# Performance work log

Hardware: AMD Instinct MI355X
Metric: run time of the kernel (lower is better)

Reference implementation:

```python
import jax, jax.numpy as jnp
import numpy as np

B, C, T = 8, 1024, 2048
CI = C // 2
BN_EPS = 1e-5


def setup_inputs() -> dict:
    key = jax.random.key(0)
    ks = jax.random.split(key, 12)
    sc_in = 1.0 / np.sqrt(C)
    sc_ci = 1.0 / np.sqrt(CI)
    return {
        "x": jax.random.normal(ks[0], (B, C, T), dtype=jnp.float32),
        "Wq_w": jax.random.normal(ks[1], (CI, C), dtype=jnp.float32) * sc_in,
        "Wq_b": jax.random.normal(ks[2], (CI,), dtype=jnp.float32) * 0.02,
        "Wk_w": jax.random.normal(ks[3], (CI, C), dtype=jnp.float32) * sc_in,
        "Wk_b": jax.random.normal(ks[4], (CI,), dtype=jnp.float32) * 0.02,
        "Wv_w": jax.random.normal(ks[5], (CI, C), dtype=jnp.float32) * sc_in,
        "Wv_b": jax.random.normal(ks[6], (CI,), dtype=jnp.float32) * 0.02,
        "Wo_w": jax.random.normal(ks[7], (C, CI), dtype=jnp.float32) * sc_ci,
        "Wo_b": jax.random.normal(ks[8], (C,), dtype=jnp.float32) * 0.02,
        "gamma": jax.random.normal(ks[9], (C,), dtype=jnp.float32) * 0.1 + 1.0,
        "beta": jax.random.normal(ks[10], (C,), dtype=jnp.float32) * 0.02,
    }


def reference(x, Wq_w, Wq_b, Wk_w, Wk_b, Wv_w, Wv_b, Wo_w, Wo_b, gamma, beta):
    # 1x1 Conv1d projections == channel-wise linear maps
    q = jnp.einsum('oc,bct->bto', Wq_w, x) + Wq_b          # [B, T, Ci]
    k = jnp.einsum('oc,bct->bot', Wk_w, x) + Wk_b[:, None]  # [B, Ci, T]
    v = jnp.einsum('oc,bct->bto', Wv_w, x) + Wv_b          # [B, T, Ci]

    s = jnp.einsum('bqc,bck->bqk', q, k)                   # [B, Tq, Tk], unscaled
    sim = jax.nn.softmax(s, axis=-2)                        # softmax over QUERY axis
    y = jnp.einsum('bqk,bkc->bcq', sim, v)                  # [B, Ci, T]

    wy = jnp.einsum('oc,bct->bot', Wo_w, y) + Wo_b[:, None]  # [B, C, T]

    # BatchNorm1d in training mode: stats over (batch, time) per channel
    mean = jnp.mean(wy, axis=(0, 2), keepdims=True)
    var = jnp.var(wy, axis=(0, 2), keepdims=True)
    wy_bn = (wy - mean) * jax.lax.rsqrt(var + BN_EPS)
    wy_bn = wy_bn * gamma[None, :, None] + beta[None, :, None]

    return wy_bn + x
```

## Files before the change

kernel.cpp:

```cpp
#include <hip/hip_runtime.h>
#include <hip/hip_fp16.h>

typedef _Float16 f16;
typedef f16 f16x8 __attribute__((ext_vector_type(8)));
typedef f16 f16x4 __attribute__((ext_vector_type(4)));
typedef float f32x4 __attribute__((ext_vector_type(4)));

constexpr int Bb = 8, Cc = 1024, Tt = 2048, Ci = 512;
constexpr float BN_EPS = 1e-5f;

__device__ __forceinline__ void gload16(const f16* g, f16* l) {
  __builtin_amdgcn_global_load_lds(
      (const __attribute__((address_space(1))) void*)g,
      (__attribute__((address_space(3))) void*)l, 16, 0, 0);
}

__global__ __launch_bounds__(256)
void cvt_kernel(const float* __restrict__ src, f16* __restrict__ dst, int n4) {
  int i = blockIdx.x * blockDim.x + threadIdx.x;
  if (i < n4) {
    float4 v = *((const float4*)src + i);
    f16x4 h;
    h[0] = (f16)v.x; h[1] = (f16)v.y; h[2] = (f16)v.z; h[3] = (f16)v.w;
    *((f16x4*)dst + i) = h;
  }
}

__global__ __launch_bounds__(256)
void cvtT_kernel(const float* __restrict__ x, f16* __restrict__ xT) {
  __shared__ float tile[64][68];
  const int b = blockIdx.z, c0 = blockIdx.y * 64, t0 = blockIdx.x * 64;
  const int tid = threadIdx.x;
  const float* xp = x + ((long)b * Cc + c0) * Tt + t0;
  {
    int r = tid >> 4, c4 = (tid & 15) * 4;
    #pragma unroll
    for (int it = 0; it < 4; it++) {
      float4 v = *(const float4*)(xp + (long)(r + it * 16) * Tt + c4);
      *(float4*)&tile[r + it * 16][c4] = v;
    }
  }
  __syncthreads();
  f16* op = xT + ((long)b * Tt + t0) * Cc + c0;
  {
    int c8 = (tid & 7) * 8;
    #pragma unroll
    for (int it = 0; it < 2; it++) {
      int t = (tid >> 3) + it * 32;
      f16x8 o;
      #pragma unroll
      for (int jj = 0; jj < 8; jj++) o[jj] = (f16)tile[c8 + jj][t];
      *(f16x8*)(op + (long)t * Cc + c8) = o;
    }
  }
}

template<int BIAS_MODE, bool DO_MAX>
__global__ __launch_bounds__(512, 2)
void gemm8p(const f16* __restrict__ A, const f16* __restrict__ B,
            f16* __restrict__ C, const float* __restrict__ bias,
            unsigned* __restrict__ gmax,
            int K, int lda, int ldb, int ldc, long sA, long sB, long sC,
            int nx, int ny)
{
  extern __shared__ f16 lds[];
  constexpr int TILE_A = 256 * 32;
  constexpr int TILE_B = 128 * 32;
  constexpr int TILE   = TILE_A + TILE_B;

  const int per = gridDim.x >> 3;
  const int nid = (blockIdx.x & 7) * per + (blockIdx.x >> 3);
  const int bz = nid / (nx * ny);
  const int rem = nid - bz * nx * ny;
  const int by = rem / nx, bx = rem - by * nx;

  const int tid = threadIdx.x, lane = tid & 63, wv = tid >> 6;
  const int bm0 = by * 256, bn0 = bx * 128;
  const int wm = (wv >> 1) * 64, wn = (wv & 1) * 64;
  const f16* Ab = A + (long)bz * sA + (long)bm0 * lda;
  const f16* Bt = B + (long)bz * sB + (long)bn0 * ldb;
  C += (long)bz * sC;

  const int r16 = lane & 15, khi = lane >> 4;

  auto stA = [&](int slot, int k0, int r) {
    int L = (r * 512 + tid) * 16;
    int G = L ^ (((L >> 7) & 3) << 4);
    gload16(Ab + (long)(G >> 6) * lda + k0 + ((G & 63) >> 1),
            lds + (long)slot * TILE + (r * 512 + wv * 64) * 8);
  };
  auto stB = [&](int slot, int k0) {
    int L = tid * 16;
    int G = L ^ (((L >> 7) & 3) << 4);
    gload16(Bt + (long)(G >> 6) * ldb + k0 + ((G & 63) >> 1),
            lds + (long)slot * TILE + TILE_A + (wv * 64) * 8);
  };

  f32x4 acc[4][4] = {};
  const int nt = K >> 5;

  stA(0, 0, 0); stA(0, 0, 1); stB(0, 0);
  stA(1, 32, 0); stA(1, 32, 1); stB(1, 32);
  asm volatile("s_waitcnt vmcnt(3)" ::: "memory");
  __builtin_amdgcn_s_barrier();

  for (int t = 0; t < nt; t++) {
    const int slot = t % 3;
    const int nslot = (t + 2) % 3;
    const int k2 = (t + 2) << 5;
    const bool st = (t + 2) < nt;
    const char* baseA = (const char*)(lds + (long)slot * TILE);
    const char* baseB = (const char*)(lds + (long)slot * TILE + TILE_A);

    if (st) { stA(nslot, k2, 0); stA(nslot, k2, 1); stB(nslot, k2); }

    f16x8 af[4], bf[4];
    #pragma unroll
    for (int i = 0; i < 4; i++) {
      const int row = wm + i * 16 + r16;
      af[i] = *(const f16x8*)(baseA + (((row << 6) + (khi << 4)) ^ (((row >> 1) & 3) << 4)));
    }
    #pragma unroll
    for (int j = 0; j < 4; j++) {
      const int row = wn + j * 16 + r16;
      bf[j] = *(const f16x8*)(baseB + (((row << 6) + (khi << 4)) ^ (((row >> 1) & 3) << 4)));
    }

    __builtin_amdgcn_s_setprio(1);
    #pragma unroll
    for (int i = 0; i < 4; i++)
      #pragma unroll
      for (int j = 0; j < 4; j++)
        acc[i][j] = __builtin_amdgcn_mfma_f32_16x16x32_f16(af[i], bf[j], acc[i][j], 0, 0, 0);
    __builtin_amdgcn_s_setprio(0);

    __builtin_amdgcn_sched_barrier(0);
    if (st) asm volatile("s_waitcnt vmcnt(3)" ::: "memory");
    else    asm volatile("s_waitcnt vmcnt(0)" ::: "memory");
    __builtin_amdgcn_s_barrier();
  }

  const int rg = khi * 4;
  float cmx[4] = {-3e38f, -3e38f, -3e38f, -3e38f};
  #pragma unroll
  for (int i = 0; i < 4; i++) {
    const int row0 = bm0 + wm + i * 16 + rg;
    #pragma unroll
    for (int r = 0; r < 4; r++) {
      const int row = row0 + r;
      const float br = (BIAS_MODE == 1) ? bias[row] : 0.0f;
      #pragma unroll
      for (int j = 0; j < 4; j++) {
        const int col = bn0 + wn + j * 16 + r16;
        float v = acc[i][j][r] + ((BIAS_MODE == 2) ? bias[col] : br);
        C[(long)row * ldc + col] = (f16)v;
        if (DO_MAX) cmx[j] = fmaxf(cmx[j], v);
      }
    }
  }
  if (DO_MAX) {
    #pragma unroll
    for (int j = 0; j < 4; j++) {
      float mx = cmx[j];
      mx = fmaxf(mx, __shfl_xor(mx, 16));
      mx = fmaxf(mx, __shfl_xor(mx, 32));
      if (khi == 0) {
        const int col = bn0 + wn + j * 16 + r16;
        unsigned u = __float_as_uint(mx);
        unsigned key = (u & 0x80000000u) ? ~u : (u | 0x80000000u);
        atomicMax(gmax + (long)bz * ldc + col, key);
      }
    }
  }
}

__global__ __launch_bounds__(256)
void colsum_kernel(f16* __restrict__ E, const unsigned* __restrict__ gmax,
                   float* __restrict__ sums) {
  const int b = blockIdx.z;
  const int kt = blockIdx.x * 256 + threadIdx.x;
  const long q0 = (long)blockIdx.y * 128;
  unsigned key = gmax[b * Tt + kt];
  float m = (key & 0x80000000u) ? __uint_as_float(key ^ 0x80000000u)
                                : __uint_as_float(~key);
  f16* p = E + ((long)b * Tt + q0) * Tt + kt;
  float s = 0.f;
  #pragma unroll 4
  for (int q = 0; q < 128; q++) {
    float e = __expf((float)p[(long)q * Tt] - m);
    p[(long)q * Tt] = (f16)e;
    s += e;
  }
  atomicAdd(sums + b * Tt + kt, s);
}

__global__ __launch_bounds__(256)
void vscale_kernel(f16* __restrict__ Vt, const float* __restrict__ sums) {
  long i = ((long)blockIdx.x * 256 + threadIdx.x) * 8;
  int kt = (int)(i & (Tt - 1));
  int b = (int)(i >> 20);
  f16x8 v = *(f16x8*)(Vt + i);
  const float* sp = sums + b * Tt + kt;
  #pragma unroll
  for (int j = 0; j < 8; j++)
    v[j] = (f16)((float)v[j] * __fdividef(1.0f, sp[j]));
  *(f16x8*)(Vt + i) = v;
}

__global__ __launch_bounds__(256)
void bnstat_kernel(const f16* __restrict__ wy, float* __restrict__ bsum,
                   float* __restrict__ bsq) {
  const int c = blockIdx.x, tid = threadIdx.x;
  float s1 = 0.f, s2 = 0.f;
  for (int b = 0; b < Bb; b++) {
    f16x8 v = *((const f16x8*)(wy + ((long)b * Cc + c) * Tt) + tid);
    #pragma unroll
    for (int jj = 0; jj < 8; jj++) { float f = (float)v[jj]; s1 += f; s2 += f * f; }
  }
  #pragma unroll
  for (int off = 1; off < 64; off <<= 1) {
    s1 += __shfl_xor(s1, off);
    s2 += __shfl_xor(s2, off);
  }
  __shared__ float l1[4], l2[4];
  const int w = tid >> 6;
  if ((tid & 63) == 0) { l1[w] = s1; l2[w] = s2; }
  __syncthreads();
  if (tid == 0) {
    bsum[c] = (l1[0] + l1[1]) + (l1[2] + l1[3]);
    bsq[c]  = (l2[0] + l2[1]) + (l2[2] + l2[3]);
  }
}

__global__ __launch_bounds__(256)
void final_kernel(const f16* __restrict__ wy, const float* __restrict__ x,
                  const float* __restrict__ gamma, const float* __restrict__ beta,
                  const float* __restrict__ bsum, const float* __restrict__ bsq,
                  float* __restrict__ out)
{
  long i = ((long)blockIdx.x * blockDim.x + threadIdx.x) * 4;
  int c = (int)((i >> 11) & (Cc - 1));
  const float cnt = (float)Bb * (float)Tt;
  float mean = bsum[c] / cnt;
  float var  = bsq[c] / cnt - mean * mean;
  float sc = rsqrtf(var + BN_EPS) * gamma[c];
  float sh = beta[c] - mean * sc;
  f16x4 w = *(const f16x4*)(wy + i);
  float4 xv = *(const float4*)(x + i);
  float4 o;
  o.x = (float)w[0] * sc + sh + xv.x;
  o.y = (float)w[1] * sc + sh + xv.y;
  o.z = (float)w[2] * sc + sh + xv.z;
  o.w = (float)w[3] * sc + sh + xv.w;
  *(float4*)(out + i) = o;
}

extern "C" void kernel_launch(void* const* d_in, const int* in_sizes, int n_in,
                              void* d_out, int out_size, void* d_ws, size_t ws_size,
                              hipStream_t stream) {
  const float* x    = (const float*)d_in[0];
  const float* Wq_w = (const float*)d_in[1];
  const float* Wq_b = (const float*)d_in[2];
  const float* Wk_w = (const float*)d_in[3];
  const float* Wk_b = (const float*)d_in[4];
  const float* Wv_w = (const float*)d_in[5];
  const float* Wv_b = (const float*)d_in[6];
  const float* Wo_w = (const float*)d_in[7];
  const float* Wo_b = (const float*)d_in[8];
  const float* gamma = (const float*)d_in[9];
  const float* beta  = (const float*)d_in[10];
  float* out = (float*)d_out;

  constexpr long SZ_XT = (long)Bb * Tt * Cc;
  constexpr long SZ_Q  = (long)Bb * Tt * Ci;
  constexpr long SZ_S  = (long)Bb * Tt * Tt;
  constexpr long SZ_W  = (long)Ci * Cc;

  f16* ws = (f16*)d_ws;
  f16* xT  = ws;
  f16* QK  = xT + SZ_XT;
  f16* Vt  = QK + SZ_XT;
  f16* Sq  = Vt + SZ_Q;
  f16* Y   = Sq + SZ_S;
  f16* wy  = Y + SZ_Q;
  f16* wqk = wy + SZ_XT;
  f16* wv  = wqk + 2 * SZ_W;
  f16* wo  = wv + SZ_W;
  unsigned* gmax = (unsigned*)(wo + SZ_W);
  float* sums = (float*)(gmax + (long)Bb * Tt);
  float* bsum = sums + (long)Bb * Tt;
  float* bsq  = bsum + Cc;
  float* qkb  = bsq + Cc;

  constexpr int LDSB = (256 * 32 + 128 * 32) * 3 * 2;
  hipFuncSetAttribute(reinterpret_cast<const void*>(gemm8p<2, false>),
                      hipFuncAttributeMaxDynamicSharedMemorySize, LDSB);
  hipFuncSetAttribute(reinterpret_cast<const void*>(gemm8p<1, false>),
                      hipFuncAttributeMaxDynamicSharedMemorySize, LDSB);
  hipFuncSetAttribute(reinterpret_cast<const void*>(gemm8p<0, true>),
                      hipFuncAttributeMaxDynamicSharedMemorySize, LDSB);
  hipFuncSetAttribute(reinterpret_cast<const void*>(gemm8p<0, false>),
                      hipFuncAttributeMaxDynamicSharedMemorySize, LDSB);

  hipMemsetAsync(gmax, 0, (long)Bb * Tt * 2 * sizeof(float), stream);
  hipMemcpyAsync(qkb, Wq_b, Ci * sizeof(float), hipMemcpyDeviceToDevice, stream);
  hipMemcpyAsync(qkb + Ci, Wk_b, Ci * sizeof(float), hipMemcpyDeviceToDevice, stream);

  cvt_kernel<<<(int)(SZ_W / 4 / 256), 256, 0, stream>>>(Wq_w, wqk, (int)(SZ_W / 4));
  cvt_kernel<<<(int)(SZ_W / 4 / 256), 256, 0, stream>>>(Wk_w, wqk + SZ_W, (int)(SZ_W / 4));
  cvt_kernel<<<(int)(SZ_W / 4 / 256), 256, 0, stream>>>(Wv_w, wv, (int)(SZ_W / 4));
  cvt_kernel<<<(int)(SZ_W / 4 / 256), 256, 0, stream>>>(Wo_w, wo, (int)(SZ_W / 4));
  cvtT_kernel<<<dim3(Tt / 64, Cc / 64, Bb), 256, 0, stream>>>(x, xT);

  gemm8p<2, false><<<8 * 8 * Bb, 512, LDSB, stream>>>(
      xT, wqk, QK, qkb, nullptr,
      Cc, Cc, Cc, 1024, (long)Tt * Cc, 0, (long)Tt * 1024, 8, 8);

  gemm8p<1, false><<<16 * 2 * Bb, 512, LDSB, stream>>>(
      wv, xT, Vt, Wv_b, nullptr,
      Cc, Cc, Cc, Tt, 0, (long)Tt * Cc, (long)Ci * Tt, 16, 2);

  gemm8p<0, true><<<16 * 8 * Bb, 512, LDSB, stream>>>(
      QK, QK + 512, Sq, nullptr, gmax,
      Ci, 1024, 1024, Tt, (long)Tt * 1024, (long)Tt * 1024, (long)Tt * Tt, 16, 8);

  colsum_kernel<<<dim3(Tt / 256, Tt / 128, Bb), 256, 0, stream>>>(Sq, gmax, sums);

  vscale_kernel<<<(int)(SZ_Q / 8 / 256), 256, 0, stream>>>(Vt, sums);

  gemm8p<0, false><<<4 * 8 * Bb, 512, LDSB, stream>>>(
      Sq, Vt, Y, nullptr, nullptr,
      Tt, Tt, Tt, Ci, (long)Tt * Tt, (long)Ci * Tt, (long)Tt * Ci, 4, 8);

  gemm8p<1, false><<<16 * 4 * Bb, 512, LDSB, stream>>>(
      wo, Y, wy, Wo_b, nullptr,
      Ci, Ci, Ci, Tt, 0, (long)Tt * Ci, (long)Cc * Tt, 16, 4);

  bnstat_kernel<<<Cc, 256, 0, stream>>>(wy, bsum, bsq);
  final_kernel<<<(int)(SZ_XT / 4 / 256), 256, 0, stream>>>(
      wy, x, gamma, beta, bsum, bsq, out);
}
```

Measured before the change: 271.7 us.

## Add 256x256-tile GEMM variant for QK projection, scores and output projection

Introduces a new GEMM kernel with 256x256 block tiles (8 waves, each 128x64), a two-buffer LDS pipeline with interleaved loads and MFMA phases, and prioritised MFMA issue. It replaces the 256x128-tile kernel for the QK projection, the QK^T score GEMM (with column max), and the output projection, halving the grid sizes. Larger tiles raise arithmetic intensity and cut global/LDS traffic per FLOP, at the cost of 128KB LDS per block, a larger accumulator register footprint, and fewer blocks, which could hurt occupancy and load balance.

```diff
diff --git a/kernel.cpp b/kernel.cpp
--- a/kernel.cpp
+++ b/kernel.cpp
@@ -51,6 +51,145 @@
       #pragma unroll
       for (int jj = 0; jj < 8; jj++) o[jj] = (f16)tile[c8 + jj][t];
       *(f16x8*)(op + (long)t * Cc + c8) = o;
+    }
+  }
+}
+
+template<int BIAS_MODE, bool DO_MAX>
+__global__ __launch_bounds__(512, 2)
+void gemm8ph(const f16* __restrict__ A, const f16* __restrict__ B,
+             f16* __restrict__ C, const float* __restrict__ bias,
+             unsigned* __restrict__ gmax,
+             int K, int lda, int ldb, int ldc, long sA, long sB, long sC,
+             int nx, int ny)
+{
+  extern __shared__ f16 lds[];
+  const int per = gridDim.x >> 3;
+  const int nid = (blockIdx.x & 7) * per + (blockIdx.x >> 3);
+  const int bz = nid / (nx * ny);
+  const int rem = nid - bz * nx * ny;
+  const int by = rem / nx, bx = rem - by * nx;
+
+  const int tid = threadIdx.x, lane = tid & 63, wv = tid >> 6;
+  const int bm0 = by * 256, bn0 = bx * 256;
+  const int wm = wv >> 2, wn = wv & 3;
+  const f16* Ab = A + (long)bz * sA + (long)bm0 * lda;
+  const f16* Bt = B + (long)bz * sB + (long)bn0 * ldb;
+  C += (long)bz * sC;
+  const int r16 = lane & 15, khl = lane >> 4;
+
+  auto stA = [&](int buf, int ks, int k0) {
+    #pragma unroll
+    for (int r = 0; r < 2; r++) {
+      int id = r * 512 + tid;
+      gload16(Ab + (long)(id & 255) * lda + k0 + ks * 32 + (id >> 8) * 8,
+              lds + buf * 32768 + ks * 8192 + (r * 512 + wv * 64) * 8);
+    }
+  };
+  auto stB = [&](int buf, int ks, int k0) {
+    #pragma unroll
+    for (int r = 0; r < 2; r++) {
+      int id = r * 512 + tid;
+      gload16(Bt + (long)(id & 255) * ldb + k0 + ks * 32 + (id >> 8) * 8,
+              lds + buf * 32768 + 16384 + ks * 8192 + (r * 512 + wv * 64) * 8);
+    }
+  };
+
+  const int aB = khl * 2048 + (wm * 128 + r16) * 8;
+  const int bB = 16384 + khl * 2048 + (wn * 64 + r16) * 8;
+
+  f32x4 acc[8][4] = {};
+  const int ni = K >> 7;
+
+  stA(0, 0, 0); stB(0, 0, 0); stA(0, 1, 0); stB(0, 1, 0);
+  stA(1, 0, 64); stB(1, 0, 64);
+  asm volatile("s_waitcnt vmcnt(4)" ::: "memory");
+  __builtin_amdgcn_s_barrier();
+
+  f16x8 af[4], bf[4];
+
+#define RD_A(buf, ks, mi0) { _Pragma("unroll") for (int m = 0; m < 4; m++) \
+    af[m] = *(const f16x8*)(lds + (buf) * 32768 + (ks) * 8192 + aB + (mi0 + m) * 128); }
+#define RD_B(buf, ks) { _Pragma("unroll") for (int n = 0; n < 4; n++) \
+    bf[n] = *(const f16x8*)(lds + (buf) * 32768 + (ks) * 8192 + bB + n * 128); }
+#define BAR1 __builtin_amdgcn_s_barrier(); \
+    asm volatile("s_waitcnt lgkmcnt(0)" ::: "memory"); \
+    __builtin_amdgcn_sched_barrier(0);
+#define MM(mi0) __builtin_amdgcn_s_setprio(1); \
+    { _Pragma("unroll") for (int m = 0; m < 4; m++) { _Pragma("unroll") for (int n = 0; n < 4; n++) \
+        acc[mi0 + m][n] = __builtin_amdgcn_mfma_f32_16x16x32_f16(af[m], bf[n], acc[mi0 + m][n], 0, 0, 0); } } \
+    __builtin_amdgcn_s_setprio(0);
+#define BAR2 __builtin_amdgcn_s_barrier();
+
+  for (int i = 0; i < ni; i++) {
+    const int k1 = (2 * i + 1) << 6, k2 = (2 * i + 2) << 6, k3 = (2 * i + 3) << 6;
+    const bool more = (i + 1) < ni;
+    RD_A(0, 0, 0); RD_B(0, 0);
+    stA(1, 1, k1);
+    BAR1; MM(0); BAR2;
+    RD_A(0, 0, 4);
+    stB(1, 1, k1);
+    BAR1; MM(4); BAR2;
+    RD_A(0, 1, 0); RD_B(0, 1);
+    if (more) stA(0, 0, k2);
+    BAR1; MM(0); BAR2;
+    RD_A(0, 1, 4);
+    if (more) stB(0, 0, k2);
+    BAR1; MM(4);
+    if (more) asm volatile("s_waitcnt vmcnt(4)" ::: "memory");
+    else      asm volatile("s_waitcnt vmcnt(0)" ::: "memory");
+    BAR2;
+    RD_A(1, 0, 0); RD_B(1, 0);
+    if (more) stA(0, 1, k2);
+    BAR1; MM(0); BAR2;
+    RD_A(1, 0, 4);
+    if (more) stB(0, 1, k2);
+    BAR1; MM(4); BAR2;
+    RD_A(1, 1, 0); RD_B(1, 1);
+    if (more) stA(1, 0, k3);
+    BAR1; MM(0); BAR2;
+    RD_A(1, 1, 4);
+    if (more) stB(1, 0, k3);
+    BAR1; MM(4);
+    if (more) asm volatile("s_waitcnt vmcnt(4)" ::: "memory");
+    BAR2;
+  }
+#undef RD_A
+#undef RD_B
+#undef BAR1
+#undef MM
+#undef BAR2
+
+  const int rg = khl * 4;
+  float cmx[4] = {-3e38f, -3e38f, -3e38f, -3e38f};
+  #pragma unroll
+  for (int mi = 0; mi < 8; mi++) {
+    const int row0 = bm0 + wm * 128 + mi * 16 + rg;
+    #pragma unroll
+    for (int r = 0; r < 4; r++) {
+      const int row = row0 + r;
+      const float br = (BIAS_MODE == 1) ? bias[row] : 0.0f;
+      #pragma unroll
+      for (int nj = 0; nj < 4; nj++) {
+        const int col = bn0 + wn * 64 + nj * 16 + r16;
+        float v = acc[mi][nj][r] + ((BIAS_MODE == 2) ? bias[col] : br);
+        C[(long)row * ldc + col] = (f16)v;
+        if (DO_MAX) cmx[nj] = fmaxf(cmx[nj], v);
+      }
+    }
+  }
+  if (DO_MAX) {
+    #pragma unroll
+    for (int nj = 0; nj < 4; nj++) {
+      float mx = cmx[nj];
+      mx = fmaxf(mx, __shfl_xor(mx, 16));
+      mx = fmaxf(mx, __shfl_xor(mx, 32));
+      if (khl == 0) {
+        const int col = bn0 + wn * 64 + nj * 16 + r16;
+        unsigned u = __float_as_uint(mx);
+        unsigned key = (u & 0x80000000u) ? ~u : (u | 0x80000000u);
+        atomicMax(gmax + (long)bz * ldc + col, key);
+      }
     }
   }
 }
@@ -292,12 +431,15 @@
   float* bsq  = bsum + Cc;
   float* qkb  = bsq + Cc;
 
-  constexpr int LDSB = (256 * 32 + 128 * 32) * 3 * 2;
-  hipFuncSetAttribute(reinterpret_cast<const void*>(gemm8p<2, false>),
-                      hipFuncAttributeMaxDynamicSharedMemorySize, LDSB);
+  constexpr int LDSB  = (256 * 32 + 128 * 32) * 3 * 2;
+  constexpr int LDSB8 = 2 * 32768 * 2;
+  hipFuncSetAttribute(reinterpret_cast<const void*>(gemm8ph<2, false>),
+                      hipFuncAttributeMaxDynamicSharedMemorySize, LDSB8);
+  hipFuncSetAttribute(reinterpret_cast<const void*>(gemm8ph<1, false>),
+                      hipFuncAttributeMaxDynamicSharedMemorySize, LDSB8);
+  hipFuncSetAttribute(reinterpret_cast<const void*>(gemm8ph<0, true>),
+                      hipFuncAttributeMaxDynamicSharedMemorySize, LDSB8);
   hipFuncSetAttribute(reinterpret_cast<const void*>(gemm8p<1, false>),
-                      hipFuncAttributeMaxDynamicSharedMemorySize, LDSB);
-  hipFuncSetAttribute(reinterpret_cast<const void*>(gemm8p<0, true>),
                       hipFuncAttributeMaxDynamicSharedMemorySize, LDSB);
   hipFuncSetAttribute(reinterpret_cast<const void*>(gemm8p<0, false>),
                       hipFuncAttributeMaxDynamicSharedMemorySize, LDSB);
@@ -312,17 +454,17 @@
   cvt_kernel<<<(int)(SZ_W / 4 / 256), 256, 0, stream>>>(Wo_w, wo, (int)(SZ_W / 4));
   cvtT_kernel<<<dim3(Tt / 64, Cc / 64, Bb), 256, 0, stream>>>(x, xT);
 
-  gemm8p<2, false><<<8 * 8 * Bb, 512, LDSB, stream>>>(
+  gemm8ph<2, false><<<4 * 8 * Bb, 512, LDSB8, stream>>>(
       xT, wqk, QK, qkb, nullptr,
-      Cc, Cc, Cc, 1024, (long)Tt * Cc, 0, (long)Tt * 1024, 8, 8);
+      Cc, Cc, Cc, 1024, (long)Tt * Cc, 0, (long)Tt * 1024, 4, 8);
 
   gemm8p<1, false><<<16 * 2 * Bb, 512, LDSB, stream>>>(
       wv, xT, Vt, Wv_b, nullptr,
       Cc, Cc, Cc, Tt, 0, (long)Tt * Cc, (long)Ci * Tt, 16, 2);
 
-  gemm8p<0, true><<<16 * 8 * Bb, 512, LDSB, stream>>>(
+  gemm8ph<0, true><<<8 * 8 * Bb, 512, LDSB8, stream>>>(
       QK, QK + 512, Sq, nullptr, gmax,
-      Ci, 1024, 1024, Tt, (long)Tt * 1024, (long)Tt * 1024, (long)Tt * Tt, 16, 8);
+      Ci, 1024, 1024, Tt, (long)Tt * 1024, (long)Tt * 1024, (long)Tt * Tt, 8, 8);
 
   colsum_kernel<<<dim3(Tt / 256, Tt / 128, Bb), 256, 0, stream>>>(Sq, gmax, sums);
 
@@ -332,9 +474,9 @@
       Sq, Vt, Y, nullptr, nullptr,
       Tt, Tt, Tt, Ci, (long)Tt * Tt, (long)Ci * Tt, (long)Tt * Ci, 4, 8);
 
-  gemm8p<1, false><<<16 * 4 * Bb, 512, LDSB, stream>>>(
+  gemm8ph<1, false><<<8 * 4 * Bb, 512, LDSB8, stream>>>(
       wo, Y, wy, Wo_b, nullptr,
-      Ci, Ci, Ci, Tt, 0, (long)Tt * Ci, (long)Cc * Tt, 16, 4);
+      Ci, Ci, Ci, Tt, 0, (long)Tt * Ci, (long)Cc * Tt, 8, 4);
 
   bnstat_kernel<<<Cc, 256, 0, stream>>>(wy, bsum, bsq);
   final_kernel<<<(int)(SZ_XT / 4 / 256), 256, 0, stream>>>(
```

New measurement: 298.9 us. +10.0%, slower.

## Fuse BN statistics into output GEMM epilogue, vectorize colsum, merge weight casts

Applied to the files above, without the earlier changes.

The output projection GEMM epilogue now accumulates per-row sums and sums of squares into LDS and writes per-tile partials. A small reduce kernel combines them, replacing the bnstat pass that re-read the whole wy tensor. The exp/column-sum kernel now handles 8 columns per thread with 16-byte vector loads and stores. The four weight fp16 conversions become one launch. The costs are extra shuffles and LDS atomics in the GEMM epilogue, slightly more LDS per block, and reusing the xT buffer for the partials.

```diff
diff --git a/kernel.cpp b/kernel.cpp
--- a/kernel.cpp
+++ b/kernel.cpp
@@ -16,14 +16,16 @@
 }
 
 __global__ __launch_bounds__(256)
-void cvt_kernel(const float* __restrict__ src, f16* __restrict__ dst, int n4) {
-  int i = blockIdx.x * blockDim.x + threadIdx.x;
-  if (i < n4) {
-    float4 v = *((const float4*)src + i);
-    f16x4 h;
-    h[0] = (f16)v.x; h[1] = (f16)v.y; h[2] = (f16)v.z; h[3] = (f16)v.w;
-    *((f16x4*)dst + i) = h;
-  }
+void cvt4_kernel(const float* __restrict__ s0, const float* __restrict__ s1,
+                 const float* __restrict__ s2, const float* __restrict__ s3,
+                 f16* __restrict__ dst) {
+  const float* srcs[4] = {s0, s1, s2, s3};
+  const int region = blockIdx.x >> 9;
+  const int i = (blockIdx.x & 511) * 256 + threadIdx.x;
+  float4 v = *((const float4*)srcs[region] + i);
+  f16x4 h;
+  h[0] = (f16)v.x; h[1] = (f16)v.y; h[2] = (f16)v.z; h[3] = (f16)v.w;
+  *((f16x4*)dst + (long)region * 131072 + i) = h;
 }
 
 __global__ __launch_bounds__(256)
@@ -55,11 +57,12 @@
   }
 }
 
-template<int BIAS_MODE, bool DO_MAX>
+template<int BIAS_MODE, bool DO_MAX, bool DO_BN>
 __global__ __launch_bounds__(512, 2)
 void gemm8p(const f16* __restrict__ A, const f16* __restrict__ B,
             f16* __restrict__ C, const float* __restrict__ bias,
             unsigned* __restrict__ gmax,
+            float* __restrict__ part1, float* __restrict__ part2,
             int K, int lda, int ldb, int ldc, long sA, long sB, long sC,
             int nx, int ny)
 {
@@ -82,6 +85,10 @@
   C += (long)bz * sC;
 
   const int r16 = lane & 15, khi = lane >> 4;
+
+  float* lsum = (float*)(lds + 3 * TILE);
+  float* lsq  = lsum + 256;
+  if (DO_BN && tid < 256) { lsum[tid] = 0.f; lsq[tid] = 0.f; }
 
   auto stA = [&](int slot, int k0, int r) {
     int L = (r * 512 + tid) * 16;
@@ -149,12 +156,26 @@
     for (int r = 0; r < 4; r++) {
       const int row = row0 + r;
       const float br = (BIAS_MODE == 1) ? bias[row] : 0.0f;
+      float s1 = 0.f, s2 = 0.f;
       #pragma unroll
       for (int j = 0; j < 4; j++) {
         const int col = bn0 + wn + j * 16 + r16;
         float v = acc[i][j][r] + ((BIAS_MODE == 2) ? bias[col] : br);
         C[(long)row * ldc + col] = (f16)v;
         if (DO_MAX) cmx[j] = fmaxf(cmx[j], v);
+        if (DO_BN) { s1 += v; s2 += v * v; }
+      }
+      if (DO_BN) {
+        #pragma unroll
+        for (int off = 1; off < 16; off <<= 1) {
+          s1 += __shfl_xor(s1, off);
+          s2 += __shfl_xor(s2, off);
+        }
+        if (r16 == 0) {
+          const int rowl = wm + i * 16 + rg + r;
+          atomicAdd(&lsum[rowl], s1);
+          atomicAdd(&lsq[rowl], s2);
+        }
       }
     }
   }
@@ -172,26 +193,45 @@
       }
     }
   }
+  if (DO_BN) {
+    __syncthreads();
+    if (tid < 256) {
+      const long idx = ((long)bz * (ny * 256) + bm0 + tid) * nx + bx;
+      part1[idx] = lsum[tid];
+      part2[idx] = lsq[tid];
+    }
+  }
 }
 
 __global__ __launch_bounds__(256)
 void colsum_kernel(f16* __restrict__ E, const unsigned* __restrict__ gmax,
                    float* __restrict__ sums) {
   const int b = blockIdx.z;
-  const int kt = blockIdx.x * 256 + threadIdx.x;
-  const long q0 = (long)blockIdx.y * 128;
-  unsigned key = gmax[b * Tt + kt];
-  float m = (key & 0x80000000u) ? __uint_as_float(key ^ 0x80000000u)
-                                : __uint_as_float(~key);
-  f16* p = E + ((long)b * Tt + q0) * Tt + kt;
-  float s = 0.f;
+  const int kt0 = threadIdx.x * 8;
+  const long q0 = (long)blockIdx.y * 64;
+  float m[8], s[8];
+  #pragma unroll
+  for (int j = 0; j < 8; j++) {
+    unsigned key = gmax[b * Tt + kt0 + j];
+    m[j] = (key & 0x80000000u) ? __uint_as_float(key ^ 0x80000000u)
+                               : __uint_as_float(~key);
+    s[j] = 0.f;
+  }
+  f16* p = E + ((long)b * Tt + q0) * Tt + kt0;
   #pragma unroll 4
-  for (int q = 0; q < 128; q++) {
-    float e = __expf((float)p[(long)q * Tt] - m);
-    p[(long)q * Tt] = (f16)e;
-    s += e;
-  }
-  atomicAdd(sums + b * Tt + kt, s);
+  for (int q = 0; q < 64; q++) {
+    f16x8 v = *(f16x8*)(p + (long)q * Tt);
+    f16x8 o;
+    #pragma unroll
+    for (int j = 0; j < 8; j++) {
+      float e = __expf((float)v[j] - m[j]);
+      o[j] = (f16)e;
+      s[j] += e;
+    }
+    *(f16x8*)(p + (long)q * Tt) = o;
+  }
+  #pragma unroll
+  for (int j = 0; j < 8; j++) atomicAdd(sums + b * Tt + kt0 + j, s[j]);
 }
 
 __global__ __launch_bounds__(256)
@@ -207,29 +247,21 @@
   *(f16x8*)(Vt + i) = v;
 }
 
-__global__ __launch_bounds__(256)
-void bnstat_kernel(const f16* __restrict__ wy, float* __restrict__ bsum,
-                   float* __restrict__ bsq) {
-  const int c = blockIdx.x, tid = threadIdx.x;
-  float s1 = 0.f, s2 = 0.f;
-  for (int b = 0; b < Bb; b++) {
-    f16x8 v = *((const f16x8*)(wy + ((long)b * Cc + c) * Tt) + tid);
-    #pragma unroll
-    for (int jj = 0; jj < 8; jj++) { float f = (float)v[jj]; s1 += f; s2 += f * f; }
-  }
+__global__ __launch_bounds__(64)
+void bnreduce_kernel(const float* __restrict__ part1,
+                     const float* __restrict__ part2,
+                     float* __restrict__ bsum, float* __restrict__ bsq) {
+  const int c = blockIdx.x, t = threadIdx.x;
+  const long i0 = ((long)(t >> 4) * Cc + c) * 16 + (t & 15);
+  const long i1 = ((long)((t + 64) >> 4) * Cc + c) * 16 + ((t + 64) & 15);
+  float s1 = part1[i0] + part1[i1];
+  float s2 = part2[i0] + part2[i1];
   #pragma unroll
   for (int off = 1; off < 64; off <<= 1) {
     s1 += __shfl_xor(s1, off);
     s2 += __shfl_xor(s2, off);
   }
-  __shared__ float l1[4], l2[4];
-  const int w = tid >> 6;
-  if ((tid & 63) == 0) { l1[w] = s1; l2[w] = s2; }
-  __syncthreads();
-  if (tid == 0) {
-    bsum[c] = (l1[0] + l1[1]) + (l1[2] + l1[3]);
-    bsq[c]  = (l2[0] + l2[1]) + (l2[2] + l2[3]);
-  }
+  if (t == 0) { bsum[c] = s1; bsq[c] = s2; }
 }
 
 __global__ __launch_bounds__(256)
@@ -291,52 +323,54 @@
   float* bsum = sums + (long)Bb * Tt;
   float* bsq  = bsum + Cc;
   float* qkb  = bsq + Cc;
-
-  constexpr int LDSB = (256 * 32 + 128 * 32) * 3 * 2;
-  hipFuncSetAttribute(reinterpret_cast<const void*>(gemm8p<2, false>),
+  float* part1 = (float*)xT;
+  float* part2 = part1 + (long)Bb * Cc * 16;
+
+  constexpr int LDSB    = (256 * 32 + 128 * 32) * 3 * 2;
+  constexpr int LDSB_BN = LDSB + 256 * 2 * 4;
+  hipFuncSetAttribute(reinterpret_cast<const void*>(gemm8p<2, false, false>),
                       hipFuncAttributeMaxDynamicSharedMemorySize, LDSB);
-  hipFuncSetAttribute(reinterpret_cast<const void*>(gemm8p<1, false>),
+  hipFuncSetAttribute(reinterpret_cast<const void*>(gemm8p<1, false, false>),
                       hipFuncAttributeMaxDynamicSharedMemorySize, LDSB);
-  hipFuncSetAttribute(reinterpret_cast<const void*>(gemm8p<0, true>),
+  hipFuncSetAttribute(reinterpret_cast<const void*>(gemm8p<0, true, false>),
                       hipFuncAttributeMaxDynamicSharedMemorySize, LDSB);
-  hipFuncSetAttribute(reinterpret_cast<const void*>(gemm8p<0, false>),
+  hipFuncSetAttribute(reinterpret_cast<const void*>(gemm8p<0, false, false>),
                       hipFuncAttributeMaxDynamicSharedMemorySize, LDSB);
+  hipFuncSetAttribute(reinterpret_cast<const void*>(gemm8p<1, false, true>),
+                      hipFuncAttributeMaxDynamicSharedMemorySize, LDSB_BN);
 
   hipMemsetAsync(gmax, 0, (long)Bb * Tt * 2 * sizeof(float), stream);
   hipMemcpyAsync(qkb, Wq_b, Ci * sizeof(float), hipMemcpyDeviceToDevice, stream);
   hipMemcpyAsync(qkb + Ci, Wk_b, Ci * sizeof(float), hipMemcpyDeviceToDevice, stream);
 
-  cvt_kernel<<<(int)(SZ_W / 4 / 256), 256, 0, stream>>>(Wq_w, wqk, (int)(SZ_W / 4));
-  cvt_kernel<<<(int)(SZ_W / 4 / 256), 256, 0, stream>>>(Wk_w, wqk + SZ_W, (int)(SZ_W / 4));
-  cvt_kernel<<<(int)(SZ_W / 4 / 256), 256, 0, stream>>>(Wv_w, wv, (int)(SZ_W / 4));
-  cvt_kernel<<<(int)(SZ_W / 4 / 256), 256, 0, stream>>>(Wo_w, wo, (int)(SZ_W / 4));
+  cvt4_kernel<<<2048, 256, 0, stream>>>(Wq_w, Wk_w, Wv_w, Wo_w, wqk);
   cvtT_kernel<<<dim3(Tt / 64, Cc / 64, Bb), 256, 0, stream>>>(x, xT);
 
-  gemm8p<2, false><<<8 * 8 * Bb, 512, LDSB, stream>>>(
-      xT, wqk, QK, qkb, nullptr,
+  gemm8p<2, false, false><<<8 * 8 * Bb, 512, LDSB, stream>>>(
+      xT, wqk, QK, qkb, nullptr, nullptr, nullptr,
       Cc, Cc, Cc, 1024, (long)Tt * Cc, 0, (long)Tt * 1024, 8, 8);
 
-  gemm8p<1, false><<<16 * 2 * Bb, 512, LDSB, stream>>>(
-      wv, xT, Vt, Wv_b, nullptr,
+  gemm8p<1, false, false><<<16 * 2 * Bb, 512, LDSB, stream>>>(
+      wv, xT, Vt, Wv_b, nullptr, nullptr, nullptr,
       Cc, Cc, Cc, Tt, 0, (long)Tt * Cc, (long)Ci * Tt, 16, 2);
 
-  gemm8p<0, true><<<16 * 8 * Bb, 512, LDSB, stream>>>(
-      QK, QK + 512, Sq, nullptr, gmax,
+  gemm8p<0, true, false><<<16 * 8 * Bb, 512, LDSB, stream>>>(
+      QK, QK + 512, Sq, nullptr, gmax, nullptr, nullptr,
       Ci, 1024, 1024, Tt, (long)Tt * 1024, (long)Tt * 1024, (long)Tt * Tt, 16, 8);
 
-  colsum_kernel<<<dim3(Tt / 256, Tt / 128, Bb), 256, 0, stream>>>(Sq, gmax, sums);
+  colsum_kernel<<<dim3(1, Tt / 64, Bb), 256, 0, stream>>>(Sq, gmax, sums);
 
   vscale_kernel<<<(int)(SZ_Q / 8 / 256), 256, 0, stream>>>(Vt, sums);
 
-  gemm8p<0, false><<<4 * 8 * Bb, 512, LDSB, stream>>>(
-      Sq, Vt, Y, nullptr, nullptr,
+  gemm8p<0, false, false><<<4 * 8 * Bb, 512, LDSB, stream>>>(
+      Sq, Vt, Y, nullptr, nullptr, nullptr, nullptr,
       Tt, Tt, Tt, Ci, (long)Tt * Tt, (long)Ci * Tt, (long)Tt * Ci, 4, 8);
 
-  gemm8p<1, false><<<16 * 4 * Bb, 512, LDSB, stream>>>(
-      wo, Y, wy, Wo_b, nullptr,
+  gemm8p<1, false, true><<<16 * 4 * Bb, 512, LDSB_BN, stream>>>(
+      wo, Y, wy, Wo_b, nullptr, part1, part2,
       Ci, Ci, Ci, Tt, 0, (long)Tt * Ci, (long)Cc * Tt, 16, 4);
 
-  bnstat_kernel<<<Cc, 256, 0, stream>>>(wy, bsum, bsq);
+  bnreduce_kernel<<<Cc, 64, 0, stream>>>(part1, part2, bsum, bsq);
   final_kernel<<<(int)(SZ_XT / 4 / 256), 256, 0, stream>>>(
       wy, x, gamma, beta, bsum, bsq, out);
 }
```

New measurement: 280.7 us. 1.03x slower.
